# Performance work log

Hardware: AMD Instinct MI355X
Metric: run time of the kernel (lower is better)

Reference implementation:

```python
import jax, jax.numpy as jnp
import numpy as np

P1 = np.array([[1000.0, 0.0, 128.0, 64000.0],
               [0.0, 1000.0, 128.0, 64000.0],
               [0.0, 0.0, 1.0, 500.0]])
P2 = np.array([[-128.0, 0.0, 1000.0, 64000.0],
               [-128.0, 1000.0, 0.0, 64000.0],
               [-1.0, 0.0, 0.0, 500.0]])


def calculate_fundamental_matrix(P_src, P_dst):
    # l2 = F21 @ x1 : maps a point in P_src onto a line in P_dst
    C1 = -np.linalg.inv(P_src[:3, :3]) @ P_src[:3, 3]
    e = P_dst @ np.append(C1, 1.0)          # epipole of src camera center in dst view
    return np.cross(e, np.eye(3) * -1) @ P_dst @ np.linalg.pinv(P_src)


def setup_inputs() -> dict:
    key = jax.random.key(0)
    view1 = jax.random.normal(key, (8, 4, 256, 256), dtype=jnp.float32)
    F21 = calculate_fundamental_matrix(P1, P2).astype(np.float32)
    return {"view1": view1, "F": jnp.asarray(F21)}


def reference(view1, F):
    """Epipolar image translation: out(x2) = line integral of view1 along the
    epipolar line l1 = F^T @ x2 (bilinear sampling in v, unit steps in u,
    zero outside the image). Matches fume_torch_lib.translate semantics."""
    B, C, H, W = view1.shape
    dt = view1.dtype
    F = F.astype(dt)
    ys = jnp.arange(H, dtype=dt)[:, None]   # (H,1)
    xs = jnp.arange(W, dtype=dt)[None, :]   # (1,W)
    # line coefficients l = F^T @ [x, y, 1], per output pixel -> (H,W)
    a = F[0, 0] * xs + F[1, 0] * ys + F[2, 0]
    b = F[0, 1] * xs + F[1, 1] * ys + F[2, 1]
    c = F[0, 2] * xs + F[1, 2] * ys + F[2, 2]
    n = jnp.sqrt(a * a + b * b) + jnp.asarray(1e-12, dt)
    a, b, c = a / n, b / n, c / n
    ok = (jnp.abs(b) > 1e-6).astype(dt)                 # drop near-vertical lines
    b_safe = jnp.where(jnp.abs(b) > 1e-6, b, jnp.asarray(1.0, dt))

    def step(acc, u):
        uf = u.astype(dt)
        v = -(a * uf + c) / b_safe                      # (H,W) source row per out pixel
        v0 = jnp.floor(v)
        f = v - v0
        i0 = v0.astype(jnp.int32)
        i1 = i0 + 1
        m0 = ((i0 >= 0) & (i0 < H)).astype(dt)
        m1 = ((i1 >= 0) & (i1 < H)).astype(dt)
        col = jax.lax.dynamic_index_in_dim(view1, u, axis=3, keepdims=False)  # (B,C,H)
        s0 = col[:, :, jnp.clip(i0, 0, H - 1)]          # (B,C,H,W)
        s1 = col[:, :, jnp.clip(i1, 0, H - 1)]
        val = (s0 * (1.0 - f) * m0 + s1 * f * m1) * ok
        return acc + val, None

    out, _ = jax.lax.scan(step, jnp.zeros_like(view1), jnp.arange(W))
    return out
```

## Files before the change

kernel.cpp:

```cpp
#include <hip/hip_runtime.h>
#include <cstdint>

constexpr int Hh = 256, Ww = 256, BCc = 32;

constexpr int RBLK = 35;
constexpr int USTRIDE = RBLK * BCc * 8 * 2;
constexpr int UPLANES = 264;

constexpr int DW2    = 140;
constexpr int UROW2  = DW2 * BCc * 4;
constexpr size_t PSIZE = (size_t)UPLANES * UROW2;
constexpr size_t T5_BYTES = 2 * PSIZE;

typedef _Float16 half2v   __attribute__((ext_vector_type(2)));
typedef _Float16 half8v   __attribute__((ext_vector_type(8)));
typedef __fp16   fp16x2   __attribute__((ext_vector_type(2)));
typedef float    float16v __attribute__((ext_vector_type(16)));
typedef uint32_t uint4v   __attribute__((ext_vector_type(4)));

static __device__ inline half2v pack2(float a, float b) {
    fp16x2 r = __builtin_amdgcn_cvt_pkrtz(a, b);
    return __builtin_bit_cast(half2v, r);
}

__global__ __launch_bounds__(256) void fume_pack2(const float* __restrict__ in,
                                                  char* __restrict__ P) {
    const int t   = threadIdx.x;
    const int bid = blockIdx.x;
    const int rt  = bid % 18;
    const int ut  = bid / 18;
    const int R0  = rt * 16;
    const int u0  = ut * 16;
    __shared__ float lds[32][17][17];

    for (int idx = t; idx < 32 * 17 * 16; idx += 256) {
        int ch  = idx / (17 * 16);
        int rem = idx - ch * (17 * 16);
        int rl  = rem >> 4;
        int uu  = rem & 15;
        int r   = R0 + rl - 8;
        int u   = u0 + uu;
        float v = 0.f;
        if ((unsigned)r < 256u && u < 256)
            v = in[ch * (Hh * Ww) + r * Ww + u];
        lds[ch][rl][uu] = v;
    }
    __syncthreads();

    for (int w = t; w < 8192; w += 256) {
        int ch    = w & 31;
        int rest  = w >> 5;
        int uu    = rest & 15;
        int rest2 = rest >> 4;
        int dd    = rest2 & 7;
        int p     = rest2 >> 3;
        int d     = (R0 >> 1) + dd;
        int u     = u0 + uu;
        if (d >= DW2 || u >= UPLANES) continue;
        int rl = 2 * dd + p;
        half2v pr = pack2(lds[ch][rl][uu], lds[ch][rl + 1][uu]);
        uint32_t wv;
        __builtin_memcpy(&wv, &pr, 4);
        *(uint32_t*)(P + (size_t)p * PSIZE + (size_t)u * UROW2
                     + d * 128 + ch * 4) = wv;
    }
}

__global__ __launch_bounds__(256, 4) void fume_mfma2(const char* __restrict__ P,
                                                     const float* __restrict__ Fm,
                                                     float* __restrict__ out) {
    __shared__ float red[4][32][33];
    const int t    = threadIdx.x;
    const int lane = t & 63;
    const int wq   = t >> 6;
    const int px   = lane & 31;
    const int h    = lane >> 5;
    const int bid  = (int)blockIdx.x;
    const int idx8 = bid >> 3;
    const int y    = ((bid & 7) << 5) + (idx8 >> 3);
    const int x0   = (idx8 & 7) * 32;
    const int x    = x0 + px;

    float xf = (float)x, yf = (float)y;
    float a = Fm[0] * xf + Fm[3] * yf + Fm[6];
    float b = Fm[1] * xf + Fm[4] * yf + Fm[7];
    float c = Fm[2] * xf + Fm[5] * yf + Fm[8];
    float n = sqrtf(a * a + b * b) + 1e-12f;
    a /= n; b /= n; c /= n;

    float alpha, beta_i;
    int u_lo, u_hi;
    if (fabsf(b) > 1e-6f) {
        alpha  = -a / b;
        beta_i = -c / b + 8.f;
        u_lo = 0; u_hi = Ww - 1;
        if (fabsf(alpha) > 1e-12f) {
            float inv = 1.f / alpha;
            float t0 = (7.f - beta_i) * inv;
            float t1 = (264.f - beta_i) * inv;
            int lo = (int)floorf(fminf(t0, t1));
            int hi = (int)ceilf (fmaxf(t0, t1));
            u_lo = lo > 0 ? lo : 0;
            u_hi = hi < (Ww - 1) ? hi : (Ww - 1);
        } else if (beta_i <= 7.f || beta_i >= 264.f) {
            u_lo = 1 << 20; u_hi = -(1 << 20);
        }
    } else {
        alpha = 0.f; beta_i = 3.0e4f;
        u_lo = 1 << 20; u_hi = -(1 << 20);
    }

    float xA = (float)x0, xB = (float)(x0 + 31);
    float aA = Fm[0] * xA + Fm[3] * yf + Fm[6];
    float bA = Fm[1] * xA + Fm[4] * yf + Fm[7];
    float cA = Fm[2] * xA + Fm[5] * yf + Fm[8];
    float aB = Fm[0] * xB + Fm[3] * yf + Fm[6];
    float bB = Fm[1] * xB + Fm[4] * yf + Fm[7];
    float cB = Fm[2] * xB + Fm[5] * yf + Fm[8];
    float alA = -aA / bA, beA = -cA / bA + 8.f;
    float alB = -aB / bB, beB = -cB / bB + 8.f;

    int lo = u_lo, hi = u_hi;
#pragma unroll
    for (int off = 1; off < 64; off <<= 1) {
        int l2 = __shfl_xor(lo, off, 64);
        int h2 = __shfl_xor(hi, off, 64);
        lo = lo < l2 ? lo : l2;
        hi = hi > h2 ? hi : h2;
    }
    lo = __builtin_amdgcn_readfirstlane(lo);
    hi = __builtin_amdgcn_readfirstlane(hi);

    float16v acc = {0.f, 0.f, 0.f, 0.f, 0.f, 0.f, 0.f, 0.f,
                    0.f, 0.f, 0.f, 0.f, 0.f, 0.f, 0.f, 0.f};

    if (lo <= hi) {
        int len = hi - lo + 1;
        int C   = (len + 3) >> 2;
        int cq  = (C + 3) >> 2;
        int nit = C - wq * cq;
        nit = nit < 0 ? 0 : (nit > cq ? cq : nit);
        int npair = nit << 1;
        int us  = lo + wq * cq * 4;

        int   u_l = us + lane;
        float uf  = (float)u_l;
        float vAl = fmaf(alA, uf, beA);
        float vBl = fmaf(alB, uf, beB);
        float mnu = fminf(vAl, vBl);
        float Mff = floorf(mnu - 0.01f);
        Mff = fmaxf(0.f, fminf(Mff, 272.f));
        int   Mi   = (int)Mff;
        int   pb   = Mi & 1;
        int   vOff = (pb ? (int)PSIZE : 0) + u_l * UROW2 + (Mi >> 1) * 128;
        int   vMfB = __builtin_bit_cast(int, Mff);

        float alpha2 = alpha + alpha;
        float vhh = fmaf(alpha, (float)(us + h), beta_i);
        const int h4  = h << 2;
        const int chb = px << 2;

        const half2v one2 = {(_Float16)1.f, (_Float16)1.f};

#define FUME_PAIR(T)                                                          \
    do {                                                                      \
        int baddr = ((T) << 3) + h4;                                          \
        int offv  = __builtin_amdgcn_ds_bpermute(baddr, vOff);                \
        float mf  = __builtin_bit_cast(                                       \
            float, __builtin_amdgcn_ds_bpermute(baddr, vMfB));                \
        const char* q = P + (unsigned)(offv + chb);                           \
        uint32_t b0 = *(const uint32_t*)(q);                                  \
        uint32_t b1 = *(const uint32_t*)(q + 128);                            \
        uint32_t b2 = *(const uint32_t*)(q + 256);                            \
        uint32_t b3 = *(const uint32_t*)(q + 384);                            \
        float vbl = vhh - mf;                                                 \
        half2v vb2 = pack2(vbl, vbl);                                         \
        uint32_t aw[4];                                                       \
        _Pragma("unroll")                                                     \
        for (int j_ = 0; j_ < 4; ++j_) {                                      \
            half2v cj = {(_Float16)(float)(2 * j_),                           \
                         (_Float16)(float)(2 * j_ + 1)};                      \
            half2v d_  = vb2 - cj;                                            \
            uint32_t du;                                                      \
            __builtin_memcpy(&du, &d_, 4);                                    \
            du &= 0x7fff7fffu;                                                \
            half2v ad;                                                        \
            __builtin_memcpy(&ad, &du, 4);                                    \
            half2v tj;                                                        \
            asm("v_pk_add_f16 %0, %1, %2 neg_lo:[0,1] neg_hi:[0,1] clamp"     \
                : "=v"(tj)                                                    \
                : "v"(one2), "v"(ad));                                        \
            __builtin_memcpy(&aw[j_], &tj, 4);                                \
        }                                                                     \
        half8v A;                                                             \
        __builtin_memcpy(&A, aw, 16);                                         \
        uint4v bw = {b0, b1, b2, b3};                                         \
        half8v B = __builtin_bit_cast(half8v, bw);                            \
        acc = __builtin_amdgcn_mfma_f32_32x32x16_f16(A, B, acc, 0, 0, 0);     \
        vhh += alpha2;                                                        \
    } while (0)

        for (int tp = 0; tp < npair; tp += 2) {
            FUME_PAIR(tp);
            FUME_PAIR(tp + 1);
        }
#undef FUME_PAIR
    }

#pragma unroll
    for (int r = 0; r < 16; ++r) {
        int m = (r & 3) + 8 * (r >> 2) + 4 * h;
        red[wq][m][px] = acc[r];
    }
    __syncthreads();
    {
        int pxs = t & 31, cg = t >> 5;
#pragma unroll
        for (int jj = 0; jj < 4; ++jj) {
            int ch = cg + 8 * jj;
            float val = red[0][pxs][ch] + red[1][pxs][ch]
                      + red[2][pxs][ch] + red[3][pxs][ch];
            out[(size_t)ch * (Hh * Ww) + y * Ww + x0 + pxs] = val;
        }
    }
}

__global__ __launch_bounds__(256) void fume_pack(const float* __restrict__ in,
                                                 char* __restrict__ T4) {
    const int t   = threadIdx.x;
    const int bid = blockIdx.x;
    if (bid >= 512) {
        constexpr int NA = UPLANES * 3 * 32;
        constexpr int NB = 8 * 32 * 32;
        for (int id = (bid - 512) * 256 + t; id < NA + NB; id += 8 * 256) {
            int u, blk, ch;
            if (id < NA) {
                u = id / 96;
                int rem = id - u * 96;
                int bsel = rem >> 5;
                blk = (bsel == 0) ? 0 : (bsel == 1 ? 33 : 34);
                ch = rem & 31;
            } else {
                int id2 = id - NA;
                u = 256 + (id2 >> 10);
                int rem = id2 & 1023;
                blk = 1 + (rem >> 5);
                ch = rem & 31;
            }
            uint4v z = {0, 0, 0, 0};
            *(uint4v*)(T4 + (size_t)u * USTRIDE + blk * 512 + ch * 16) = z;
        }
        return;
    }
    __shared__ float lds[8][8][65];
    const int chg = bid & 3;
    const int r0  = ((bid >> 2) & 31) * 8;
    const int u0  = (bid >> 7) * 64;
    const int blk = (r0 >> 3) + 1;

#pragma unroll
    for (int it = 0; it < 16; ++it) {
        int idx = it * 256 + t;
        int ch = idx >> 9, rr = (idx >> 6) & 7, uu = idx & 63;
        lds[ch][rr][uu] =
            in[(chg * 8 + ch) * (Hh * Ww) + (r0 + rr) * Ww + u0 + uu];
    }
    __syncthreads();
    const int chl = t & 7;
#pragma unroll
    for (int p = 0; p < 2; ++p) {
        int u_l = (t >> 3) + p * 32;
        uint32_t w[4];
#pragma unroll
        for (int j = 0; j < 4; ++j) {
            half2v pr = pack2(lds[chl][2 * j][u_l], lds[chl][2 * j + 1][u_l]);
            __builtin_memcpy(&w[j], &pr, 4);
        }
        uint4v val = {w[0], w[1], w[2], w[3]};
        *(uint4v*)(T4 + (size_t)(u0 + u_l) * USTRIDE + blk * 512
                   + (chg * 8 + chl) * 16) = val;
    }
}

__global__ __launch_bounds__(256, 4) void fume_mfma(const char* __restrict__ T4,
                                                    const float* __restrict__ Fm,
                                                    float* __restrict__ out) {
    __shared__ float red[4][32][33];
    const int t    = threadIdx.x;
    const int lane = t & 63;
    const int wq   = t >> 6;
    const int px   = lane & 31;
    const int h    = lane >> 5;
    const int bid  = (int)blockIdx.x;
    const int idx8 = bid >> 3;
    const int y    = ((bid & 7) << 5) + (idx8 >> 3);
    const int x0   = (idx8 & 7) * 32;
    const int x    = x0 + px;

    float xf = (float)x, yf = (float)y;
    float a = Fm[0] * xf + Fm[3] * yf + Fm[6];
    float b = Fm[1] * xf + Fm[4] * yf + Fm[7];
    float c = Fm[2] * xf + Fm[5] * yf + Fm[8];
    float n = sqrtf(a * a + b * b) + 1e-12f;
    a /= n; b /= n; c /= n;

    float alpha, beta_i;
    int u_lo, u_hi;
    if (fabsf(b) > 1e-6f) {
        alpha  = -a / b;
        beta_i = -c / b + 8.f;
        u_lo = 0; u_hi = Ww - 1;
        if (fabsf(alpha) > 1e-12f) {
            float inv = 1.f / alpha;
            float t0 = (7.f - beta_i) * inv;
            float t1 = (264.f - beta_i) * inv;
            int lo = (int)floorf(fminf(t0, t1));
            int hi = (int)ceilf (fmaxf(t0, t1));
            u_lo = lo > 0 ? lo : 0;
            u_hi = hi < (Ww - 1) ? hi : (Ww - 1);
        } else if (beta_i <= 7.f || beta_i >= 264.f) {
            u_lo = 1 << 20; u_hi = -(1 << 20);
        }
    } else {
        alpha = 0.f; beta_i = 3.0e4f;
        u_lo = 1 << 20; u_hi = -(1 << 20);
    }

    float xA = (float)x0, xB = (float)(x0 + 31);
    float aA = Fm[0] * xA + Fm[3] * yf + Fm[6];
    float bA = Fm[1] * xA + Fm[4] * yf + Fm[7];
    float cA = Fm[2] * xA + Fm[5] * yf + Fm[8];
    float aB = Fm[0] * xB + Fm[3] * yf + Fm[6];
    float bB = Fm[1] * xB + Fm[4] * yf + Fm[7];
    float cB = Fm[2] * xB + Fm[5] * yf + Fm[8];
    float alA = -aA / bA, beA = -cA / bA + 8.f;
    float alB = -aB / bB, beB = -cB / bB + 8.f;

    int lo = u_lo, hi = u_hi;
#pragma unroll
    for (int off = 1; off < 64; off <<= 1) {
        int l2 = __shfl_xor(lo, off, 64);
        int h2 = __shfl_xor(hi, off, 64);
        lo = lo < l2 ? lo : l2;
        hi = hi > h2 ? hi : h2;
    }
    lo = __builtin_amdgcn_readfirstlane(lo);
    hi = __builtin_amdgcn_readfirstlane(hi);

    float16v acc = {0.f, 0.f, 0.f, 0.f, 0.f, 0.f, 0.f, 0.f,
                    0.f, 0.f, 0.f, 0.f, 0.f, 0.f, 0.f, 0.f};

    if (lo <= hi) {
        int len = hi - lo + 1;
        int C   = (len + 3) >> 2;
        int cq  = (C + 3) >> 2;
        int nit = C - wq * cq;
        nit = nit < 0 ? 0 : (nit > cq ? cq : nit);
        int n4  = nit << 2;
        int us  = lo + wq * cq * 4;

        float uf  = (float)(us + lane);
        float vAl = fmaf(alA, uf, beA);
        float vBl = fmaf(alB, uf, beB);
        float mnu = fminf(vAl, vBl);
        float Mf  = floorf(fmaf(mnu, 0.125f, -0.125f));
        Mf = fmaxf(0.f, fminf(Mf, 33.f));
        int   vMo  = (int)Mf << 9;
        float vB8f = Mf * 8.f;
        int   vB8i = __builtin_bit_cast(int, vB8f);

        float l8h = (float)(8 * h);
        float vh  = fmaf(alpha, (float)us, beta_i) - l8h;
        const char* pb  = T4 + (size_t)us * USTRIDE;
        const int voff  = (h << 9) + (px << 4);

        const half2v one2 = {(_Float16)1.f, (_Float16)1.f};

        for (int it2 = 0; it2 < n4; it2 += 4) {
#pragma unroll
            for (int i = 0; i < 4; ++i) {
                const int idx = it2 + i;
                int   Mo = __builtin_amdgcn_readlane(vMo, idx);
                float b8 = __builtin_bit_cast(
                    float, __builtin_amdgcn_readlane(vB8i, idx));
                uint4v bw = *(const uint4v*)(pb + (size_t)idx * USTRIDE
                                             + (size_t)Mo + voff);
                float vbl = vh - b8;
                half2v vb2 = pack2(vbl, vbl);
                uint32_t aw[4];
#pragma unroll
                for (int j = 0; j < 4; ++j) {
                    half2v cj = {(_Float16)(float)(2 * j),
                                 (_Float16)(float)(2 * j + 1)};
                    half2v d  = vb2 - cj;
                    uint32_t du;
                    __builtin_memcpy(&du, &d, 4);
                    du &= 0x7fff7fffu;
                    half2v ad;
                    __builtin_memcpy(&ad, &du, 4);
                    half2v tj;
                    asm("v_pk_add_f16 %0, %1, %2 neg_lo:[0,1] neg_hi:[0,1] clamp"
                        : "=v"(tj)
                        : "v"(one2), "v"(ad));
                    __builtin_memcpy(&aw[j], &tj, 4);
                }
                half8v A;
                __builtin_memcpy(&A, aw, 16);
                half8v B = __builtin_bit_cast(half8v, bw);
                acc = __builtin_amdgcn_mfma_f32_32x32x16_f16(A, B, acc, 0, 0, 0);
                vh += alpha;
            }
        }
    }

#pragma unroll
    for (int r = 0; r < 16; ++r) {
        int m = (r & 3) + 8 * (r >> 2) + 4 * h;
        red[wq][m][px] = acc[r];
    }
    __syncthreads();
    {
        int pxs = t & 31, cg = t >> 5;
#pragma unroll
        for (int jj = 0; jj < 4; ++jj) {
            int ch = cg + 8 * jj;
            float val = red[0][pxs][ch] + red[1][pxs][ch]
                      + red[2][pxs][ch] + red[3][pxs][ch];
            out[(size_t)ch * (Hh * Ww) + y * Ww + x0 + pxs] = val;
        }
    }
}

__global__ __launch_bounds__(256) void fume_fallback(const float* __restrict__ src,
                                                     const float* __restrict__ Fm,
                                                     float* __restrict__ out) {
    int g = blockIdx.x * 256 + threadIdx.x;
    int part = g & 3;
    int pix  = g >> 2;
    int x = pix & (Ww - 1);
    int y = pix >> 8;
    int ch0 = part * 8;
    float xf = (float)x, yf = (float)y;
    float a = Fm[0] * xf + Fm[3] * yf + Fm[6];
    float b = Fm[1] * xf + Fm[4] * yf + Fm[7];
    float c = Fm[2] * xf + Fm[5] * yf + Fm[8];
    float n = sqrtf(a * a + b * b) + 1e-12f;
    a /= n; b /= n; c /= n;
    float acc[8];
#pragma unroll
    for (int k = 0; k < 8; ++k) acc[k] = 0.f;
    if (fabsf(b) > 1e-6f) {
        float alpha = -a / b, beta = -c / b;
        for (int u = 0; u < Ww; ++u) {
            float v  = fmaf(alpha, (float)u, beta);
            float rf = floorf(v);
            float f  = v - rf;
            int   ri = (int)rf;
            float w0 = ((unsigned)ri       < (unsigned)Hh) ? (1.f - f) : 0.f;
            float w1 = ((unsigned)(ri + 1) < (unsigned)Hh) ? f         : 0.f;
            int r0 = ri < 0 ? 0 : (ri > Hh - 1 ? Hh - 1 : ri);
            int r1 = ri + 1 < 0 ? 0 : (ri + 1 > Hh - 1 ? Hh - 1 : ri + 1);
#pragma unroll
            for (int k = 0; k < 8; ++k) {
                float s0 = src[(size_t)(ch0 + k) * (Hh * Ww) + r0 * Ww + u];
                float s1 = src[(size_t)(ch0 + k) * (Hh * Ww) + r1 * Ww + u];
                acc[k] = fmaf(w0, s0, fmaf(w1, s1, acc[k]));
            }
        }
    }
#pragma unroll
    for (int k = 0; k < 8; ++k)
        out[(size_t)(ch0 + k) * (Hh * Ww) + pix] = acc[k];
}

extern "C" void kernel_launch(void* const* d_in, const int* in_sizes, int n_in,
                              void* d_out, int out_size, void* d_ws, size_t ws_size,
                              hipStream_t stream) {
    const float* view1 = (const float*)d_in[0];
    const float* Fm    = (const float*)d_in[1];
    float* out = (float*)d_out;

    constexpr size_t t4_bytes = (size_t)UPLANES * USTRIDE;
    if (ws_size >= T5_BYTES) {
        char* P = (char*)d_ws;
        fume_pack2<<<306, 256, 0, stream>>>(view1, P);
        fume_mfma2<<<2048, 256, 0, stream>>>(P, Fm, out);
    } else if (ws_size >= t4_bytes) {
        char* T4 = (char*)d_ws;
        fume_pack<<<520, 256, 0, stream>>>(view1, T4);
        fume_mfma<<<2048, 256, 0, stream>>>(T4, Fm, out);
    } else {
        fume_fallback<<<(Hh * Ww * 4) / 256, 256, 0, stream>>>(view1, Fm, out);
    }
}
```

Baseline: 97.07 us.

## Double-buffer B-operand loads in MFMA loop and vectorize pack loads

The main MFMA kernel now issues the global loads for the next chunk of u-columns into a second register buffer while computing the current chunk. The per-pair ds_bpermute calls are replaced with scalar readlane selects. The pack kernel's global reads are widened to float4 vector loads. The intent is to hide global memory latency in the inner loop and cut LDS permute traffic, at the cost of more live registers and one redundant prefetch at the tail.

```diff
diff --git a/kernel.cpp b/kernel.cpp
--- a/kernel.cpp
+++ b/kernel.cpp
@@ -16,6 +16,7 @@
 typedef _Float16 half8v   __attribute__((ext_vector_type(8)));
 typedef __fp16   fp16x2   __attribute__((ext_vector_type(2)));
 typedef float    float16v __attribute__((ext_vector_type(16)));
+typedef float    float4v  __attribute__((ext_vector_type(4)));
 typedef uint32_t uint4v   __attribute__((ext_vector_type(4)));
 
 static __device__ inline half2v pack2(float a, float b) {
@@ -33,17 +34,20 @@
     const int u0  = ut * 16;
     __shared__ float lds[32][17][17];
 
-    for (int idx = t; idx < 32 * 17 * 16; idx += 256) {
-        int ch  = idx / (17 * 16);
-        int rem = idx - ch * (17 * 16);
-        int rl  = rem >> 4;
-        int uu  = rem & 15;
+    for (int idx = t; idx < 32 * 17 * 4; idx += 256) {
+        int q   = idx & 3;
+        int rem = idx >> 2;
+        int rl  = rem % 17;
+        int ch  = rem / 17;
         int r   = R0 + rl - 8;
-        int u   = u0 + uu;
-        float v = 0.f;
-        if ((unsigned)r < 256u && u < 256)
-            v = in[ch * (Hh * Ww) + r * Ww + u];
-        lds[ch][rl][uu] = v;
+        int uq  = u0 + q * 4;
+        float4v v = {0.f, 0.f, 0.f, 0.f};
+        if ((unsigned)r < 256u && uq < 256)
+            v = *(const float4v*)&in[ch * (Hh * Ww) + r * Ww + uq];
+        lds[ch][rl][q * 4 + 0] = v[0];
+        lds[ch][rl][q * 4 + 1] = v[1];
+        lds[ch][rl][q * 4 + 2] = v[2];
+        lds[ch][rl][q * 4 + 3] = v[3];
     }
     __syncthreads();
 
@@ -66,7 +70,7 @@
     }
 }
 
-__global__ __launch_bounds__(256, 4) void fume_mfma2(const char* __restrict__ P,
+__global__ __launch_bounds__(256, 4) void fume_mfma3(const char* __restrict__ P,
                                                      const float* __restrict__ Fm,
                                                      float* __restrict__ out) {
     __shared__ float red[4][32][33];
@@ -140,7 +144,6 @@
         int cq  = (C + 3) >> 2;
         int nit = C - wq * cq;
         nit = nit < 0 ? 0 : (nit > cq ? cq : nit);
-        int npair = nit << 1;
         int us  = lo + wq * cq * 4;
 
         int   u_l = us + lane;
@@ -157,54 +160,79 @@
 
         float alpha2 = alpha + alpha;
         float vhh = fmaf(alpha, (float)(us + h), beta_i);
-        const int h4  = h << 2;
         const int chb = px << 2;
 
         const half2v one2 = {(_Float16)1.f, (_Float16)1.f};
 
-#define FUME_PAIR(T)                                                          \
+        uint32_t bA8[8], bB8[8];
+
+#define FUME_ISS3(BUF, CH)                                                    \
     do {                                                                      \
-        int baddr = ((T) << 3) + h4;                                          \
-        int offv  = __builtin_amdgcn_ds_bpermute(baddr, vOff);                \
-        float mf  = __builtin_bit_cast(                                       \
-            float, __builtin_amdgcn_ds_bpermute(baddr, vMfB));                \
-        const char* q = P + (unsigned)(offv + chb);                           \
-        uint32_t b0 = *(const uint32_t*)(q);                                  \
-        uint32_t b1 = *(const uint32_t*)(q + 128);                            \
-        uint32_t b2 = *(const uint32_t*)(q + 256);                            \
-        uint32_t b3 = *(const uint32_t*)(q + 384);                            \
-        float vbl = vhh - mf;                                                 \
-        half2v vb2 = pack2(vbl, vbl);                                         \
-        uint32_t aw[4];                                                       \
         _Pragma("unroll")                                                     \
-        for (int j_ = 0; j_ < 4; ++j_) {                                      \
-            half2v cj = {(_Float16)(float)(2 * j_),                           \
-                         (_Float16)(float)(2 * j_ + 1)};                      \
-            half2v d_  = vb2 - cj;                                            \
-            uint32_t du;                                                      \
-            __builtin_memcpy(&du, &d_, 4);                                    \
-            du &= 0x7fff7fffu;                                                \
-            half2v ad;                                                        \
-            __builtin_memcpy(&ad, &du, 4);                                    \
-            half2v tj;                                                        \
-            asm("v_pk_add_f16 %0, %1, %2 neg_lo:[0,1] neg_hi:[0,1] clamp"     \
-                : "=v"(tj)                                                    \
-                : "v"(one2), "v"(ad));                                        \
-            __builtin_memcpy(&aw[j_], &tj, 4);                                \
+        for (int pr_ = 0; pr_ < 2; ++pr_) {                                   \
+            int li_  = (CH) * 4 + 2 * pr_;                                    \
+            int oe_  = __builtin_amdgcn_readlane(vOff, li_);                  \
+            int oo_  = __builtin_amdgcn_readlane(vOff, li_ + 1);              \
+            int sel_ = h ? oo_ : oe_;                                         \
+            const char* q_ = P + (unsigned)(sel_ + chb);                      \
+            _Pragma("unroll")                                                 \
+            for (int k_ = 0; k_ < 4; ++k_)                                    \
+                (BUF)[4 * pr_ + k_] = *(const uint32_t*)(q_ + 128 * k_);      \
         }                                                                     \
-        half8v A;                                                             \
-        __builtin_memcpy(&A, aw, 16);                                         \
-        uint4v bw = {b0, b1, b2, b3};                                         \
-        half8v B = __builtin_bit_cast(half8v, bw);                            \
-        acc = __builtin_amdgcn_mfma_f32_32x32x16_f16(A, B, acc, 0, 0, 0);     \
-        vhh += alpha2;                                                        \
     } while (0)
 
-        for (int tp = 0; tp < npair; tp += 2) {
-            FUME_PAIR(tp);
-            FUME_PAIR(tp + 1);
-        }
-#undef FUME_PAIR
+#define FUME_COMP3(BUF, CH)                                                   \
+    do {                                                                      \
+        _Pragma("unroll")                                                     \
+        for (int pr_ = 0; pr_ < 2; ++pr_) {                                   \
+            int li_ = (CH) * 4 + 2 * pr_;                                     \
+            int me_ = __builtin_amdgcn_readlane(vMfB, li_);                   \
+            int mo_ = __builtin_amdgcn_readlane(vMfB, li_ + 1);               \
+            float mf_ = __builtin_bit_cast(float, h ? mo_ : me_);             \
+            float vbl_ = vhh - mf_;                                           \
+            half2v vb2_ = pack2(vbl_, vbl_);                                  \
+            uint32_t aw_[4];                                                  \
+            _Pragma("unroll")                                                 \
+            for (int j_ = 0; j_ < 4; ++j_) {                                  \
+                half2v cj_ = {(_Float16)(float)(2 * j_),                      \
+                              (_Float16)(float)(2 * j_ + 1)};                 \
+                half2v d_  = vb2_ - cj_;                                      \
+                uint32_t du_;                                                 \
+                __builtin_memcpy(&du_, &d_, 4);                               \
+                du_ &= 0x7fff7fffu;                                           \
+                half2v ad_;                                                   \
+                __builtin_memcpy(&ad_, &du_, 4);                              \
+                half2v tj_;                                                   \
+                asm("v_pk_add_f16 %0, %1, %2 neg_lo:[0,1] neg_hi:[0,1] clamp" \
+                    : "=v"(tj_)                                               \
+                    : "v"(one2), "v"(ad_));                                   \
+                __builtin_memcpy(&aw_[j_], &tj_, 4);                          \
+            }                                                                 \
+            half8v A_;                                                        \
+            __builtin_memcpy(&A_, aw_, 16);                                   \
+            uint4v bw_ = {(BUF)[4 * pr_ + 0], (BUF)[4 * pr_ + 1],             \
+                          (BUF)[4 * pr_ + 2], (BUF)[4 * pr_ + 3]};            \
+            half8v B_ = __builtin_bit_cast(half8v, bw_);                      \
+            acc = __builtin_amdgcn_mfma_f32_32x32x16_f16(A_, B_, acc, 0, 0, 0);\
+            vhh += alpha2;                                                    \
+        }                                                                     \
+    } while (0)
+
+        if (nit > 0) {
+            FUME_ISS3(bA8, 0);
+            int cc = 0;
+            while (cc + 2 <= nit) {
+                FUME_ISS3(bB8, cc + 1);
+                FUME_COMP3(bA8, cc);
+                int pf = (cc + 2 < nit) ? cc + 2 : nit - 1;
+                FUME_ISS3(bA8, pf);
+                FUME_COMP3(bB8, cc + 1);
+                cc += 2;
+            }
+            if (cc < nit) FUME_COMP3(bA8, cc);
+        }
+#undef FUME_ISS3
+#undef FUME_COMP3
     }
 
 #pragma unroll
@@ -371,7 +399,7 @@
 
         float l8h = (float)(8 * h);
         float vh  = fmaf(alpha, (float)us, beta_i) - l8h;
-        const char* pb  = T4 + (size_t)us * USTRIDE;
+        const char* pbq = T4 + (size_t)us * USTRIDE;
         const int voff  = (h << 9) + (px << 4);
 
         const half2v one2 = {(_Float16)1.f, (_Float16)1.f};
@@ -383,7 +411,7 @@
                 int   Mo = __builtin_amdgcn_readlane(vMo, idx);
                 float b8 = __builtin_bit_cast(
                     float, __builtin_amdgcn_readlane(vB8i, idx));
-                uint4v bw = *(const uint4v*)(pb + (size_t)idx * USTRIDE
+                uint4v bw = *(const uint4v*)(pbq + (size_t)idx * USTRIDE
                                              + (size_t)Mo + voff);
                 float vbl = vh - b8;
                 half2v vb2 = pack2(vbl, vbl);
@@ -484,7 +512,7 @@
     if (ws_size >= T5_BYTES) {
         char* P = (char*)d_ws;
         fume_pack2<<<306, 256, 0, stream>>>(view1, P);
-        fume_mfma2<<<2048, 256, 0, stream>>>(P, Fm, out);
+        fume_mfma3<<<2048, 256, 0, stream>>>(P, Fm, out);
     } else if (ws_size >= t4_bytes) {
         char* T4 = (char*)d_ws;
         fume_pack<<<520, 256, 0, stream>>>(view1, T4);
```

New measurement: 92.27 us. -4.9%, faster.
